# Kernel optimization log

Hardware: AMD Instinct MI355X
Metric: run time of the kernel (lower is better)

Reference implementation:

```python
import jax, jax.numpy as jnp
import numpy as np

B, S, D, H, E, K = 2, 1024, 1024, 4096, 8, 2
HE = 4 * D  # expert FFN inner dim
LN_EPS = 1e-5


def layernorm(x, g, b):
    m = x.mean(-1, keepdims=True)
    v = ((x - m) ** 2).mean(-1, keepdims=True)
    return (x - m) * jax.lax.rsqrt(v + LN_EPS) * g + b


def pos_encoding(S, D):
    pos = jnp.arange(S, dtype=jnp.float32)[:, None]
    i = jnp.arange(0, D, 2, dtype=jnp.float32)
    div = jnp.exp(-(jnp.log(10000.0)) * i / D)
    pe = jnp.zeros((S, D), dtype=jnp.float32)
    pe = pe.at[:, 0::2].set(jnp.sin(pos * div))
    pe = pe.at[:, 1::2].set(jnp.cos(pos * div))
    return pe


def setup_inputs() -> dict:
    key = jax.random.key(0)
    ks = jax.random.split(key, 16)
    w = lambda k, sh, s=0.02: (jax.random.normal(k, sh, dtype=jnp.float32) * s)
    return {
        "x": jax.random.normal(ks[0], (B, S, D), dtype=jnp.float32),
        # router: LayerNorm -> Linear(D,H) -> GELU -> Linear(H,E)
        "r_ln_g": jnp.ones((D,), jnp.float32), "r_ln_b": jnp.zeros((D,), jnp.float32),
        "r_w1": w(ks[1], (D, H)), "r_b1": jnp.zeros((H,), jnp.float32),
        "r_w2": w(ks[2], (H, E)), "r_b2": jnp.zeros((E,), jnp.float32),
        "temperature": jnp.ones((1,), jnp.float32) * 0.07,
        # stacked expert params: LayerNorm -> Linear(D,HE) -> GELU -> Linear(HE,D)
        "e_ln_g": jnp.ones((E, D), jnp.float32), "e_ln_b": jnp.zeros((E, D), jnp.float32),
        "e_w1": w(ks[3], (E, D, HE)), "e_b1": jnp.zeros((E, HE), jnp.float32),
        "e_w2": w(ks[4], (E, HE, D)), "e_b2": jnp.zeros((E, D), jnp.float32),
        # combiner: LayerNorm -> Linear(D,2D) -> GELU -> Linear(2D,D)
        "c_ln_g": jnp.ones((D,), jnp.float32), "c_ln_b": jnp.zeros((D,), jnp.float32),
        "c_w1": w(ks[5], (D, 2 * D)), "c_b1": jnp.zeros((2 * D,), jnp.float32),
        "c_w2": w(ks[6], (2 * D, D)), "c_b2": jnp.zeros((D,), jnp.float32),
        "o_ln_g": jnp.ones((D,), jnp.float32), "o_ln_b": jnp.zeros((D,), jnp.float32),
    }


def reference(x, r_ln_g, r_ln_b, r_w1, r_b1, r_w2, r_b2, temperature,
              e_ln_g, e_ln_b, e_w1, e_b1, e_w2, e_b2,
              c_ln_g, c_ln_b, c_w1, c_b1, c_w2, c_b2, o_ln_g, o_ln_b):
    gelu = lambda t: jax.nn.gelu(t, approximate=False)
    h = x + pos_encoding(S, D)[None]  # [B,S,D]
    # router logits with learned temperature
    r = layernorm(h, r_ln_g, r_ln_b)
    r = gelu(jnp.einsum("bsd,dh->bsh", r, r_w1) + r_b1)
    logits = (jnp.einsum("bsh,he->bse", r, r_w2) + r_b2) / temperature
    probs = jax.nn.softmax(logits, axis=-1)  # [B,S,E]
    topk_p, topk_i = jax.lax.top_k(probs, K)
    # sparse gate [B,S,E]: softmax prob on selected experts, 0 elsewhere
    gate = (jax.nn.one_hot(topk_i, E, dtype=probs.dtype) * topk_p[..., None]).sum(-2)
    # per-expert FFN on all tokens (dense reference of dispatch/compute/combine)
    m = h.mean(-1, keepdims=True)
    v = ((h - m) ** 2).mean(-1, keepdims=True)
    xhat = (h - m) * jax.lax.rsqrt(v + LN_EPS)  # [B,S,D], shared LN stats
    y = xhat[None] * e_ln_g[:, None, None, :] + e_ln_b[:, None, None, :]  # [E,B,S,D]
    f = gelu(jnp.einsum("ebsd,edh->ebsh", y, e_w1) + e_b1[:, None, None, :])
    f = jnp.einsum("ebsh,ehd->ebsd", f, e_w2) + e_b2[:, None, None, :]
    combined = jnp.einsum("bse,ebsd->bsd", gate, f)
    # expert combiner MLP + residual + output norm
    c = layernorm(combined, c_ln_g, c_ln_b)
    c = gelu(jnp.einsum("bsd,de->bse", c, c_w1) + c_b1)
    c = jnp.einsum("bse,ed->bsd", c, c_w2) + c_b2
    return layernorm(h + c, o_ln_g, o_ln_b)
```

## Files before the change

### kernel.cpp

```cpp
#include <hip/hip_runtime.h>
#include <stdint.h>

#define TOK 2048
#define DD  1024
#define RH  4096
#define HE  4096
#define NE  8
#define CH  2048
#define MAXTILE 40
#define MAXROWS 5120

using bf16x8 = __attribute__((ext_vector_type(8))) short;
using f32x4  = __attribute__((ext_vector_type(4))) float;

__device__ __forceinline__ unsigned short f2bf(float f) {
  union { float f; uint32_t u; } v; v.f = f;
  uint32_t r = (v.u + 0x7fffu + ((v.u >> 16) & 1u)) >> 16;
  return (unsigned short)r;
}
__device__ __forceinline__ float bf2f(unsigned short h) {
  union { uint32_t u; float f; } v; v.u = ((uint32_t)h) << 16;
  return v.f;
}
__device__ __forceinline__ float gelu_f(float x) {
  return 0.5f * x * (1.0f + erff(x * 0.70710678118654752440f));
}

#define GLD(SRC, DST) __builtin_amdgcn_global_load_lds( \
    (const __attribute__((address_space(1))) uint32_t*)(const void*)(SRC), \
    (__attribute__((address_space(3))) uint32_t*)(void*)(DST), 16, 0, 0)

__device__ __forceinline__ void block_ln_stats(float s1, float s2, float& mean, float& rstd) {
  #pragma unroll
  for (int off = 32; off > 0; off >>= 1) {
    s1 += __shfl_down(s1, off);
    s2 += __shfl_down(s2, off);
  }
  __shared__ float sh[8];
  int tid = threadIdx.x;
  if ((tid & 63) == 0) { sh[tid >> 6] = s1; sh[4 + (tid >> 6)] = s2; }
  __syncthreads();
  float t1 = sh[0] + sh[1] + sh[2] + sh[3];
  float t2 = sh[4] + sh[5] + sh[6] + sh[7];
  mean = t1 * (1.0f / 1024.0f);
  float var = t2 * (1.0f / 1024.0f) - mean * mean;
  rstd = rsqrtf(var + 1e-5f);
}

__global__ void k_prep(const float* __restrict__ x, float* __restrict__ h,
                       float* __restrict__ xh32, unsigned short* __restrict__ xhi,
                       unsigned short* __restrict__ xlo) {
  int t = blockIdx.x;
  int s = t & 1023;
  int tid = threadIdx.x;
  float4 xv = ((const float4*)(x + (size_t)t * DD))[tid];
  float v[4]; float s1 = 0.f, s2 = 0.f;
  #pragma unroll
  for (int k = 0; k < 4; ++k) {
    int d = tid * 4 + k;
    float xc = (k == 0) ? xv.x : (k == 1) ? xv.y : (k == 2) ? xv.z : xv.w;
    float i2 = (float)(d & ~1);
    float div = expf(-9.2103403719761836f * i2 * (1.0f / 1024.0f));
    float ang = (float)s * div;
    float pe = (d & 1) ? cosf(ang) : sinf(ang);
    float hv = xc + pe;
    v[k] = hv; s1 += hv; s2 += hv * hv;
  }
  float mean, rstd;
  block_ln_stats(s1, s2, mean, rstd);
  float4 ho; ho.x = v[0]; ho.y = v[1]; ho.z = v[2]; ho.w = v[3];
  ((float4*)(h + (size_t)t * DD))[tid] = ho;
  float xn[4]; unsigned short hh[4], ll[4];
  #pragma unroll
  for (int k = 0; k < 4; ++k) {
    xn[k] = (v[k] - mean) * rstd;
    hh[k] = f2bf(xn[k]);
    ll[k] = f2bf(xn[k] - bf2f(hh[k]));
  }
  float4 xo; xo.x = xn[0]; xo.y = xn[1]; xo.z = xn[2]; xo.w = xn[3];
  ((float4*)(xh32 + (size_t)t * DD))[tid] = xo;
  ushort4 h4; h4.x = hh[0]; h4.y = hh[1]; h4.z = hh[2]; h4.w = hh[3];
  ((ushort4*)(xhi + (size_t)t * DD))[tid] = h4;
  ushort4 l4; l4.x = ll[0]; l4.y = ll[1]; l4.z = ll[2]; l4.w = ll[3];
  ((ushort4*)(xlo + (size_t)t * DD))[tid] = l4;
}

__global__ void k_tconv(const float* __restrict__ in, const float* __restrict__ g,
                        unsigned short* __restrict__ out, int D, int N,
                        long long in_bs, long long g_bs, long long out_bs) {
  __shared__ float tile[32][33];
  int e = blockIdx.z;
  const float* inb = in + (size_t)e * in_bs;
  unsigned short* outb = out + (size_t)e * out_bs;
  int n0 = blockIdx.x * 32, d0 = blockIdx.y * 32;
  int tn = threadIdx.x & 31, tr = threadIdx.x >> 5;
  #pragma unroll
  for (int rr = 0; rr < 4; ++rr) {
    int dl = tr + rr * 8;
    float v = inb[(size_t)(d0 + dl) * N + n0 + tn];
    if (g) v *= g[(size_t)e * g_bs + d0 + dl];
    tile[dl][tn] = v;
  }
  __syncthreads();
  #pragma unroll
  for (int rr = 0; rr < 4; ++rr) {
    int nl = tr + rr * 8;
    outb[(size_t)(n0 + nl) * D + d0 + tn] = f2bf(tile[tn][nl]);
  }
}

__global__ void k_tconv_split(const float* __restrict__ in, const float* __restrict__ g,
                              unsigned short* __restrict__ oh, unsigned short* __restrict__ ol,
                              float* __restrict__ o32, int D, int N) {
  __shared__ float tile[32][33];
  int n0 = blockIdx.x * 32, d0 = blockIdx.y * 32;
  int tn = threadIdx.x & 31, tr = threadIdx.x >> 5;
  #pragma unroll
  for (int rr = 0; rr < 4; ++rr) {
    int dl = tr + rr * 8;
    float v = in[(size_t)(d0 + dl) * N + n0 + tn];
    if (g) v *= g[d0 + dl];
    tile[dl][tn] = v;
  }
  __syncthreads();
  #pragma unroll
  for (int rr = 0; rr < 4; ++rr) {
    int nl = tr + rr * 8;
    float v = tile[tn][nl];
    size_t off = (size_t)(n0 + nl) * D + d0 + tn;
    unsigned short hi = f2bf(v);
    oh[off] = hi;
    ol[off] = f2bf(v - bf2f(hi));
    o32[off] = v;
  }
}

__global__ void k_foldbias(const float* __restrict__ w, const float* __restrict__ lnb,
                           const float* __restrict__ b1, float* __restrict__ outb,
                           int D, int N, long long w_bs, long long lnb_bs,
                           long long b_bs, long long o_bs) {
  int e = blockIdx.y;
  int n = blockIdx.x * 256 + threadIdx.x;
  const float* wb = w + (size_t)e * w_bs;
  const float* lb = lnb + (size_t)e * lnb_bs;
  float acc = b1[(size_t)e * b_bs + n];
  for (int d = 0; d < D; ++d) {
    float l = lb[d];
    if (l != 0.f) acc += l * wb[(size_t)d * N + n];
  }
  outb[(size_t)e * o_bs + n] = acc;
}

template <int DO_GELU, int OUT_BF16>
__global__ __launch_bounds__(256)
void k_gemm(const unsigned short* __restrict__ A, const unsigned short* __restrict__ B,
            const float* __restrict__ bias, void* __restrict__ Cv, int N, int K,
            long long a_bs, long long b_bs, long long bias_bs, long long c_bs) {
  __shared__ __align__(16) unsigned short As[128 * 32];
  __shared__ __align__(16) unsigned short Bs[128 * 32];
  const int tid = threadIdx.x;
  const int w = tid >> 6, lane = tid & 63;
  const int q = lane >> 4, r16 = lane & 15;
  const int e = blockIdx.z;
  const int n0 = blockIdx.x * 128, m0 = blockIdx.y * 128;
  const unsigned short* Ab = A + (size_t)e * a_bs;
  const unsigned short* Bb = B + (size_t)e * b_bs;
  f32x4 acc[4][4];
  #pragma unroll
  for (int i = 0; i < 4; ++i)
    #pragma unroll
    for (int j = 0; j < 4; ++j) acc[i][j] = (f32x4){0.f, 0.f, 0.f, 0.f};
  const int srow = w * 32 + (lane >> 2);
  const int scol = (lane & 3) * 8;
  const unsigned short* a_src = Ab + (size_t)(m0 + srow) * K + scol;
  const unsigned short* b_src = Bb + (size_t)(n0 + srow) * K + scol;
  unsigned short* a_dst = &As[w * 1024];
  unsigned short* b_dst = &Bs[w * 1024];
  const int wm = w >> 1, wn = w & 1;
  for (int kt = 0; kt < K; kt += 32) {
    GLD(a_src + kt, a_dst);
    GLD(a_src + kt + (size_t)16 * K, a_dst + 512);
    GLD(b_src + kt, b_dst);
    GLD(b_src + kt + (size_t)16 * K, b_dst + 512);
    __syncthreads();
    bf16x8 af[4], bfv[4];
    #pragma unroll
    for (int i = 0; i < 4; ++i)
      af[i] = *(const bf16x8*)&As[(wm * 64 + i * 16 + r16) * 32 + q * 8];
    #pragma unroll
    for (int j = 0; j < 4; ++j)
      bfv[j] = *(const bf16x8*)&Bs[(wn * 64 + j * 16 + r16) * 32 + q * 8];
    #pragma unroll
    for (int i = 0; i < 4; ++i)
      #pragma unroll
      for (int j = 0; j < 4; ++j)
        acc[i][j] = __builtin_amdgcn_mfma_f32_16x16x32_bf16(af[i], bfv[j], acc[i][j], 0, 0, 0);
    __syncthreads();
  }
  #pragma unroll
  for (int j = 0; j < 4; ++j) {
    int col = n0 + wn * 64 + j * 16 + r16;
    float bv = bias[(size_t)e * bias_bs + col];
    #pragma unroll
    for (int i = 0; i < 4; ++i) {
      int row = m0 + wm * 64 + i * 16 + q * 4;
      #pragma unroll
      for (int t2 = 0; t2 < 4; ++t2) {
        float vv = acc[i][j][t2] + bv;
        if (DO_GELU) vv = gelu_f(vv);
        size_t off = (size_t)e * c_bs + (size_t)(row + t2) * N + col;
        if (OUT_BF16) ((unsigned short*)Cv)[off] = f2bf(vv);
        else ((float*)Cv)[off] = vv;
      }
    }
  }
}

__global__ __launch_bounds__(256)
void k_gemm_g1(const unsigned short* __restrict__ A, const unsigned short* __restrict__ W,
               const float* __restrict__ bias, unsigned short* __restrict__ C,
               const int* __restrict__ tok_of, const int* __restrict__ tile_e,
               const int* __restrict__ tile_r0, const int* __restrict__ ntiles) {
  if ((int)blockIdx.y >= *ntiles) return;
  __shared__ __align__(16) unsigned short As[128 * 32];
  __shared__ __align__(16) unsigned short Bs[128 * 32];
  const int tid = threadIdx.x;
  const int w = tid >> 6, lane = tid & 63;
  const int q = lane >> 4, r16 = lane & 15;
  const int e = tile_e[blockIdx.y];
  const int row0 = tile_r0[blockIdx.y];
  const int n0 = blockIdx.x * 128;
  f32x4 acc[4][4];
  #pragma unroll
  for (int i = 0; i < 4; ++i)
    #pragma unroll
    for (int j = 0; j < 4; ++j) acc[i][j] = (f32x4){0.f, 0.f, 0.f, 0.f};
  const int srow = w * 32 + (lane >> 2);
  const int scol = (lane & 3) * 8;
  const int t0 = tok_of[row0 + srow];
  const int t1 = tok_of[row0 + srow + 16];
  const unsigned short* a_src0 = A + (size_t)t0 * DD + scol;
  const unsigned short* a_src1 = A + (size_t)t1 * DD + scol;
  const unsigned short* b_src = W + (size_t)e * RH * DD + (size_t)(n0 + srow) * DD + scol;
  unsigned short* a_dst = &As[w * 1024];
  unsigned short* b_dst = &Bs[w * 1024];
  const int wm = w >> 1, wn = w & 1;
  for (int kt = 0; kt < DD; kt += 32) {
    GLD(a_src0 + kt, a_dst);
    GLD(a_src1 + kt, a_dst + 512);
    GLD(b_src + kt, b_dst);
    GLD(b_src + kt + (size_t)16 * DD, b_dst + 512);
    __syncthreads();
    bf16x8 af[4], bfv[4];
    #pragma unroll
    for (int i = 0; i < 4; ++i)
      af[i] = *(const bf16x8*)&As[(wm * 64 + i * 16 + r16) * 32 + q * 8];
    #pragma unroll
    for (int j = 0; j < 4; ++j)
      bfv[j] = *(const bf16x8*)&Bs[(wn * 64 + j * 16 + r16) * 32 + q * 8];
    #pragma unroll
    for (int i = 0; i < 4; ++i)
      #pragma unroll
      for (int j = 0; j < 4; ++j)
        acc[i][j] = __builtin_amdgcn_mfma_f32_16x16x32_bf16(af[i], bfv[j], acc[i][j], 0, 0, 0);
    __syncthreads();
  }
  #pragma unroll
  for (int j = 0; j < 4; ++j) {
    int col = n0 + wn * 64 + j * 16 + r16;
    float bv = bias[(size_t)e * RH + col];
    #pragma unroll
    for (int i = 0; i < 4; ++i) {
      int row = row0 + wm * 64 + i * 16 + q * 4;
      #pragma unroll
      for (int t2 = 0; t2 < 4; ++t2)
        C[(size_t)(row + t2) * RH + col] = f2bf(gelu_f(acc[i][j][t2] + bv));
    }
  }
}

__global__ __launch_bounds__(256)
void k_gemm_g2(const unsigned short* __restrict__ A, const unsigned short* __restrict__ W,
               unsigned short* __restrict__ C, const int* __restrict__ tile_e,
               const int* __restrict__ tile_r0, const int* __restrict__ ntiles) {
  if ((int)blockIdx.y >= *ntiles) return;
  __shared__ __align__(16) unsigned short As[128 * 32];
  __shared__ __align__(16) unsigned short Bs[128 * 32];
  const int tid = threadIdx.x;
  const int w = tid >> 6, lane = tid & 63;
  const int q = lane >> 4, r16 = lane & 15;
  const int e = tile_e[blockIdx.y];
  const int row0 = tile_r0[blockIdx.y];
  const int n0 = blockIdx.x * 128;
  f32x4 acc[4][4];
  #pragma unroll
  for (int i = 0; i < 4; ++i)
    #pragma unroll
    for (int j = 0; j < 4; ++j) acc[i][j] = (f32x4){0.f, 0.f, 0.f, 0.f};
  const int srow = w * 32 + (lane >> 2);
  const int scol = (lane & 3) * 8;
  const unsigned short* a_src = A + (size_t)(row0 + srow) * HE + scol;
  const unsigned short* b_src = W + (size_t)e * DD * HE + (size_t)(n0 + srow) * HE + scol;
  unsigned short* a_dst = &As[w * 1024];
  unsigned short* b_dst = &Bs[w * 1024];
  const int wm = w >> 1, wn = w & 1;
  for (int kt = 0; kt < HE; kt += 32) {
    GLD(a_src + kt, a_dst);
    GLD(a_src + kt + (size_t)16 * HE, a_dst + 512);
    GLD(b_src + kt, b_dst);
    GLD(b_src + kt + (size_t)16 * HE, b_dst + 512);
    __syncthreads();
    bf16x8 af[4], bfv[4];
    #pragma unroll
    for (int i = 0; i < 4; ++i)
      af[i] = *(const bf16x8*)&As[(wm * 64 + i * 16 + r16) * 32 + q * 8];
    #pragma unroll
    for (int j = 0; j < 4; ++j)
      bfv[j] = *(const bf16x8*)&Bs[(wn * 64 + j * 16 + r16) * 32 + q * 8];
    #pragma unroll
    for (int i = 0; i < 4; ++i)
      #pragma unroll
      for (int j = 0; j < 4; ++j)
        acc[i][j] = __builtin_amdgcn_mfma_f32_16x16x32_bf16(af[i], bfv[j], acc[i][j], 0, 0, 0);
    __syncthreads();
  }
  #pragma unroll
  for (int j = 0; j < 4; ++j) {
    int col = n0 + wn * 64 + j * 16 + r16;
    #pragma unroll
    for (int i = 0; i < 4; ++i) {
      int row = row0 + wm * 64 + i * 16 + q * 4;
      #pragma unroll
      for (int t2 = 0; t2 < 4; ++t2)
        C[(size_t)(row + t2) * DD + col] = f2bf(acc[i][j][t2]);
    }
  }
}

__global__ __launch_bounds__(256)
void k_gemm_split(const unsigned short* __restrict__ Ah, const unsigned short* __restrict__ Al,
                  const unsigned short* __restrict__ Bh, const unsigned short* __restrict__ Bl,
                  const float* __restrict__ bias, float* __restrict__ C, int N, int K) {
  __shared__ __align__(16) unsigned short Ahs[128 * 32];
  __shared__ __align__(16) unsigned short Als[128 * 32];
  __shared__ __align__(16) unsigned short Bhs[128 * 32];
  __shared__ __align__(16) unsigned short Bls[128 * 32];
  const int tid = threadIdx.x;
  const int w = tid >> 6, lane = tid & 63;
  const int q = lane >> 4, r16 = lane & 15;
  const int n0 = blockIdx.x * 128, m0 = blockIdx.y * 128;
  f32x4 acc[4][4];
  #pragma unroll
  for (int i = 0; i < 4; ++i)
    #pragma unroll
    for (int j = 0; j < 4; ++j) acc[i][j] = (f32x4){0.f, 0.f, 0.f, 0.f};
  const int srow = w * 32 + (lane >> 2);
  const int scol = (lane & 3) * 8;
  const unsigned short* ah_src = Ah + (size_t)(m0 + srow) * K + scol;
  const unsigned short* al_src = Al + (size_t)(m0 + srow) * K + scol;
  const unsigned short* bh_src = Bh + (size_t)(n0 + srow) * K + scol;
  const unsigned short* bl_src = Bl + (size_t)(n0 + srow) * K + scol;
  const int wm = w >> 1, wn = w & 1;
  for (int kt = 0; kt < K; kt += 32) {
    GLD(ah_src + kt, &Ahs[w * 1024]);
    GLD(ah_src + kt + (size_t)16 * K, &Ahs[w * 1024 + 512]);
    GLD(al_src + kt, &Als[w * 1024]);
    GLD(al_src + kt + (size_t)16 * K, &Als[w * 1024 + 512]);
    GLD(bh_src + kt, &Bhs[w * 1024]);
    GLD(bh_src + kt + (size_t)16 * K, &Bhs[w * 1024 + 512]);
    GLD(bl_src + kt, &Bls[w * 1024]);
    GLD(bl_src + kt + (size_t)16 * K, &Bls[w * 1024 + 512]);
    __syncthreads();
    bf16x8 ah[4], al[4], bh[4], bl[4];
    #pragma unroll
    for (int i = 0; i < 4; ++i) {
      int o = (wm * 64 + i * 16 + r16) * 32 + q * 8;
      ah[i] = *(const bf16x8*)&Ahs[o];
      al[i] = *(const bf16x8*)&Als[o];
    }
    #pragma unroll
    for (int j = 0; j < 4; ++j) {
      int o = (wn * 64 + j * 16 + r16) * 32 + q * 8;
      bh[j] = *(const bf16x8*)&Bhs[o];
      bl[j] = *(const bf16x8*)&Bls[o];
    }
    #pragma unroll
    for (int i = 0; i < 4; ++i)
      #pragma unroll
      for (int j = 0; j < 4; ++j) {
        acc[i][j] = __builtin_amdgcn_mfma_f32_16x16x32_bf16(ah[i], bh[j], acc[i][j], 0, 0, 0);
        acc[i][j] = __builtin_amdgcn_mfma_f32_16x16x32_bf16(al[i], bh[j], acc[i][j], 0, 0, 0);
        acc[i][j] = __builtin_amdgcn_mfma_f32_16x16x32_bf16(ah[i], bl[j], acc[i][j], 0, 0, 0);
      }
    __syncthreads();
  }
  #pragma unroll
  for (int j = 0; j < 4; ++j) {
    int col = n0 + wn * 64 + j * 16 + r16;
    float bv = bias[col];
    #pragma unroll
    for (int i = 0; i < 4; ++i) {
      int row = m0 + wm * 64 + i * 16 + q * 4;
      #pragma unroll
      for (int t2 = 0; t2 < 4; ++t2)
        C[(size_t)(row + t2) * N + col] = gelu_f(acc[i][j][t2] + bv);
    }
  }
}

__global__ void k_logits(const float* __restrict__ r, const float* __restrict__ w2,
                         const float* __restrict__ b2, const float* __restrict__ temp,
                         int* __restrict__ sel_i, float* __restrict__ sel_p,
                         int* __restrict__ flag, float* __restrict__ lg32) {
  int t = blockIdx.x, tid = threadIdx.x;
  const float* rr = r + (size_t)t * RH;
  float acc[NE];
  #pragma unroll
  for (int e = 0; e < NE; ++e) acc[e] = 0.f;
  #pragma unroll
  for (int k4 = 0; k4 < 4; ++k4) {
    float4 rv4 = ((const float4*)rr)[tid * 4 + k4];
    #pragma unroll
    for (int kk = 0; kk < 4; ++kk) {
      int d = tid * 16 + k4 * 4 + kk;
      float rv = (kk == 0) ? rv4.x : (kk == 1) ? rv4.y : (kk == 2) ? rv4.z : rv4.w;
      const float4* wr = (const float4*)(w2 + (size_t)d * NE);
      float4 w0 = wr[0], w1 = wr[1];
      acc[0] += rv * w0.x; acc[1] += rv * w0.y; acc[2] += rv * w0.z; acc[3] += rv * w0.w;
      acc[4] += rv * w1.x; acc[5] += rv * w1.y; acc[6] += rv * w1.z; acc[7] += rv * w1.w;
    }
  }
  #pragma unroll
  for (int off = 32; off > 0; off >>= 1)
    #pragma unroll
    for (int e = 0; e < NE; ++e) acc[e] += __shfl_down(acc[e], off);
  __shared__ float shl[4][NE];
  int w = tid >> 6, lane = tid & 63;
  if (lane == 0) {
    #pragma unroll
    for (int e = 0; e < NE; ++e) shl[w][e] = acc[e];
  }
  __syncthreads();
  if (tid == 0) {
    float tmp = temp[0];
    float lg[NE];
    #pragma unroll
    for (int e = 0; e < NE; ++e)
      lg[e] = (shl[0][e] + shl[1][e] + shl[2][e] + shl[3][e] + b2[e]) / tmp;
    float mx = lg[0];
    for (int e = 1; e < NE; ++e) mx = fmaxf(mx, lg[e]);
    float p[NE], se = 0.f;
    for (int e = 0; e < NE; ++e) { p[e] = expf(lg[e] - mx); se += p[e]; }
    float inv = 1.f / se;
    int i1 = 0; float p1 = p[0];
    for (int e = 1; e < NE; ++e) if (p[e] > p1) { p1 = p[e]; i1 = e; }
    int i2 = -1; float p2 = -1.f;
    for (int e = 0; e < NE; ++e) if (e != i1 && p[e] > p2) { p2 = p[e]; i2 = e; }
    sel_i[t * 2] = i1; sel_i[t * 2 + 1] = i2;
    sel_p[t * 2] = p1 * inv; sel_p[t * 2 + 1] = p2 * inv;
    float a1 = -1e30f, a2 = -1e30f, a3 = -1e30f;
    for (int e = 0; e < NE; ++e) {
      float vv = lg[e];
      if (vv > a1) { a3 = a2; a2 = a1; a1 = vv; }
      else if (vv > a2) { a3 = a2; a2 = vv; }
      else if (vv > a3) a3 = vv;
    }
    int fl = (a2 - a3 < 0.01f) ? 1 : 0;
    flag[t] = fl;
    if (fl) {
      #pragma unroll
      for (int e = 0; e < NE; ++e) lg32[(size_t)t * NE + e] = 0.f;
    }
  }
}

__global__ void k_triage2(const int* __restrict__ flag, const float* __restrict__ xh32,
                          const float* __restrict__ W32, const float* __restrict__ biasr,
                          const float* __restrict__ w2, float* __restrict__ lg32) {
  int t = blockIdx.y;
  if (flag[t] == 0) return;
  int tid = threadIdx.x;
  int w = tid >> 6, lane = tid & 63;
  __shared__ float xs[DD];
  ((float4*)xs)[tid] = ((const float4*)(xh32 + (size_t)t * DD))[tid];
  __syncthreads();
  int hh0 = blockIdx.x * 64 + w * 16;
  float acc[NE];
  #pragma unroll
  for (int e = 0; e < NE; ++e) acc[e] = 0.f;
  #pragma unroll
  for (int r = 0; r < 16; ++r) {
    int hh = hh0 + r;
    const float4* wrow = (const float4*)(W32 + (size_t)hh * DD);
    float s = 0.f;
    #pragma unroll
    for (int c = 0; c < 4; ++c) {
      float4 wv = wrow[lane + 64 * c];
      float4 xv = ((const float4*)xs)[lane + 64 * c];
      s += wv.x * xv.x + wv.y * xv.y + wv.z * xv.z + wv.w * xv.w;
    }
    #pragma unroll
    for (int off = 32; off > 0; off >>= 1) s += __shfl_down(s, off);
    if (lane == 0) {
      float r1 = gelu_f(s + biasr[hh]);
      const float* wr = w2 + (size_t)hh * NE;
      #pragma unroll
      for (int e = 0; e < NE; ++e) acc[e] += r1 * wr[e];
    }
  }
  __shared__ float sh2[4][NE];
  if (lane == 0) {
    #pragma unroll
    for (int e = 0; e < NE; ++e) sh2[w][e] = acc[e];
  }
  __syncthreads();
  if (tid < NE) {
    float v = sh2[0][tid] + sh2[1][tid] + sh2[2][tid] + sh2[3][tid];
    atomicAdd(&lg32[(size_t)t * NE + tid], v);
  }
}

__global__ void k_gate2(const int* __restrict__ flag, const float* __restrict__ lg32,
                        const float* __restrict__ b2, const float* __restrict__ temp,
                        int* __restrict__ sel_i, float* __restrict__ sel_p) {
  int t = blockIdx.x * 256 + threadIdx.x;
  if (t >= TOK || flag[t] == 0) return;
  float tmp = temp[0];
  float lg[NE];
  #pragma unroll
  for (int e = 0; e < NE; ++e) lg[e] = (lg32[(size_t)t * NE + e] + b2[e]) / tmp;
  float mx = lg[0];
  for (int e = 1; e < NE; ++e) mx = fmaxf(mx, lg[e]);
  float p[NE], se = 0.f;
  for (int e = 0; e < NE; ++e) { p[e] = expf(lg[e] - mx); se += p[e]; }
  float inv = 1.f / se;
  int i1 = 0; float p1 = p[0];
  for (int e = 1; e < NE; ++e) if (p[e] > p1) { p1 = p[e]; i1 = e; }
  int i2 = -1; float p2 = -1.f;
  for (int e = 0; e < NE; ++e) if (e != i1 && p[e] > p2) { p2 = p[e]; i2 = e; }
  sel_i[t * 2] = i1; sel_i[t * 2 + 1] = i2;
  sel_p[t * 2] = p1 * inv; sel_p[t * 2 + 1] = p2 * inv;
}

__global__ void k_count(const int* __restrict__ sel_i, int* __restrict__ cnt) {
  int t = blockIdx.x * 256 + threadIdx.x;
  if (t >= TOK) return;
  atomicAdd(&cnt[sel_i[2 * t]], 1);
  atomicAdd(&cnt[sel_i[2 * t + 1]], 1);
}

__global__ void k_offsets(const int* __restrict__ cnt, int* __restrict__ off,
                          int* __restrict__ tile_e, int* __restrict__ tile_r0,
                          int* __restrict__ ntiles) {
  if (threadIdx.x == 0) {
    int cur = 0, nt = 0;
    for (int e = 0; e < NE; ++e) {
      off[e] = cur;
      int n = (cnt[e] + 127) >> 7;
      for (int k = 0; k < n; ++k) { tile_e[nt] = e; tile_r0[nt] = cur + 128 * k; nt++; }
      cur += n * 128;
    }
    *ntiles = nt;
  }
}

__global__ void k_fill(const int* __restrict__ sel_i, const int* __restrict__ off,
                       int* __restrict__ fill, int* __restrict__ slotarr,
                       int* __restrict__ tok_of) {
  int t = blockIdx.x * 256 + threadIdx.x;
  if (t >= TOK) return;
  #pragma unroll
  for (int j = 0; j < 2; ++j) {
    int e = sel_i[2 * t + j];
    int pos = atomicAdd(&fill[e], 1);
    int s = off[e] + pos;
    slotarr[2 * t + j] = s;
    tok_of[s] = t;
  }
}

__global__ void k_combine2(const int* __restrict__ slotarr, const int* __restrict__ sel_i,
                           const float* __restrict__ sel_p, const unsigned short* __restrict__ pairout,
                           const float* __restrict__ e_b2, unsigned short* __restrict__ xc) {
  int t = blockIdx.x, tid = threadIdx.x;
  int s0 = slotarr[t * 2], s1 = slotarr[t * 2 + 1];
  int e0 = sel_i[t * 2], e1 = sel_i[t * 2 + 1];
  float w0 = sel_p[t * 2], w1 = sel_p[t * 2 + 1];
  ushort4 u0 = ((const ushort4*)(pairout + (size_t)s0 * DD))[tid];
  ushort4 u1 = ((const ushort4*)(pairout + (size_t)s1 * DD))[tid];
  float4 b0 = ((const float4*)(e_b2 + (size_t)e0 * DD))[tid];
  float4 b1v = ((const float4*)(e_b2 + (size_t)e1 * DD))[tid];
  float v[4];
  v[0] = w0 * (bf2f(u0.x) + b0.x) + w1 * (bf2f(u1.x) + b1v.x);
  v[1] = w0 * (bf2f(u0.y) + b0.y) + w1 * (bf2f(u1.y) + b1v.y);
  v[2] = w0 * (bf2f(u0.z) + b0.z) + w1 * (bf2f(u1.z) + b1v.z);
  v[3] = w0 * (bf2f(u0.w) + b0.w) + w1 * (bf2f(u1.w) + b1v.w);
  float s1f = v[0] + v[1] + v[2] + v[3];
  float s2f = v[0]*v[0] + v[1]*v[1] + v[2]*v[2] + v[3]*v[3];
  float mean, rstd;
  block_ln_stats(s1f, s2f, mean, rstd);
  ushort4 o;
  o.x = f2bf((v[0] - mean) * rstd); o.y = f2bf((v[1] - mean) * rstd);
  o.z = f2bf((v[2] - mean) * rstd); o.w = f2bf((v[3] - mean) * rstd);
  ((ushort4*)(xc + (size_t)t * DD))[tid] = o;
}

__global__ void k_final(const float* __restrict__ h, const unsigned short* __restrict__ c2,
                        const float* __restrict__ og, const float* __restrict__ ob,
                        float* __restrict__ out) {
  int t = blockIdx.x, tid = threadIdx.x;
  float4 hv = ((const float4*)(h + (size_t)t * DD))[tid];
  ushort4 cu = ((const ushort4*)(c2 + (size_t)t * DD))[tid];
  float v[4] = {hv.x + bf2f(cu.x), hv.y + bf2f(cu.y), hv.z + bf2f(cu.z), hv.w + bf2f(cu.w)};
  float s1 = v[0] + v[1] + v[2] + v[3];
  float s2 = v[0]*v[0] + v[1]*v[1] + v[2]*v[2] + v[3]*v[3];
  float mean, rstd;
  block_ln_stats(s1, s2, mean, rstd);
  float4 gv = ((const float4*)og)[tid];
  float4 bv = ((const float4*)ob)[tid];
  float4 o;
  o.x = (v[0] - mean) * rstd * gv.x + bv.x;
  o.y = (v[1] - mean) * rstd * gv.y + bv.y;
  o.z = (v[2] - mean) * rstd * gv.z + bv.z;
  o.w = (v[3] - mean) * rstd * gv.w + bv.w;
  ((float4*)(out + (size_t)t * DD))[tid] = o;
}

extern "C" void kernel_launch(void* const* d_in, const int* in_sizes, int n_in,
                              void* d_out, int out_size, void* d_ws, size_t ws_size,
                              hipStream_t stream) {
  (void)in_sizes; (void)n_in; (void)out_size; (void)ws_size;
  const float* x      = (const float*)d_in[0];
  const float* r_ln_g = (const float*)d_in[1];
  const float* r_ln_b = (const float*)d_in[2];
  const float* r_w1   = (const float*)d_in[3];
  const float* r_b1   = (const float*)d_in[4];
  const float* r_w2   = (const float*)d_in[5];
  const float* r_b2   = (const float*)d_in[6];
  const float* temp   = (const float*)d_in[7];
  const float* e_ln_g = (const float*)d_in[8];
  const float* e_ln_b = (const float*)d_in[9];
  const float* e_w1   = (const float*)d_in[10];
  const float* e_b1   = (const float*)d_in[11];
  const float* e_w2   = (const float*)d_in[12];
  const float* e_b2   = (const float*)d_in[13];
  const float* c_ln_g = (const float*)d_in[14];
  const float* c_ln_b = (const float*)d_in[15];
  const float* c_w1   = (const float*)d_in[16];
  const float* c_b1   = (const float*)d_in[17];
  const float* c_w2   = (const float*)d_in[18];
  const float* c_b2   = (const float*)d_in[19];
  const float* o_ln_g = (const float*)d_in[20];
  const float* o_ln_b = (const float*)d_in[21];
  float* out = (float*)d_out;

  char* base = (char*)d_ws;
  long long cur = 0;
  auto take = [&](long long sz) { char* r = base + cur; cur += (sz + 255) & ~255LL; return r; };

  float* h      = (float*)take(8388608);
  float* xh32   = (float*)take(8388608);
  unsigned short* xhi = (unsigned short*)take(4194304);
  unsigned short* xlo = (unsigned short*)take(4194304);
  unsigned short* WrH = (unsigned short*)take(8388608);
  unsigned short* WrL = (unsigned short*)take(8388608);
  float* Wr32   = (float*)take(16777216);
  float* biasr  = (float*)take(16384);
  float* ract   = (float*)take(33554432);
  int*   flag   = (int*)take(8192);
  float* lg32   = (float*)take(65536);
  int*   sel_i  = (int*)take(16384);
  float* sel_p  = (float*)take(16384);
  int*   cnt    = (int*)take(256);
  int*   off    = (int*)take(256);
  int*   fillc  = (int*)take(256);
  int*   tile_e = (int*)take(256);
  int*   tile_r0= (int*)take(256);
  int*   ntiles = (int*)take(256);
  int*   slotarr= (int*)take(16384);
  int*   tok_of = (int*)take(MAXROWS * 4);
  unsigned short* We1 = (unsigned short*)take(67108864);
  float* be1    = (float*)take(131072);
  unsigned short* We2 = (unsigned short*)take(67108864);
  unsigned short* Wc1 = (unsigned short*)take(4194304);
  float* bc1    = (float*)take(8192);
  unsigned short* Wc2 = (unsigned short*)take(4194304);
  unsigned short* xc  = (unsigned short*)take(4194304);
  unsigned short* c1  = (unsigned short*)take(8388608);
  unsigned short* c2  = (unsigned short*)take(4194304);
  unsigned short* F1g = (unsigned short*)take((long long)MAXROWS * RH * 2);
  unsigned short* pairout = (unsigned short*)take((long long)MAXROWS * DD * 2);

  hipMemsetAsync(cnt, 0, 256, stream);
  hipMemsetAsync(fillc, 0, 256, stream);
  hipMemsetAsync(tok_of, 0, MAXROWS * 4, stream);

  k_prep<<<TOK, 256, 0, stream>>>(x, h, xh32, xhi, xlo);
  k_tconv_split<<<dim3(RH/32, DD/32, 1), 256, 0, stream>>>(r_w1, r_ln_g, WrH, WrL, Wr32, DD, RH);
  k_tconv<<<dim3(RH/32, DD/32, NE), 256, 0, stream>>>(e_w1, e_ln_g, We1, DD, RH,
      (long long)DD*RH, (long long)DD, (long long)RH*DD);
  k_tconv<<<dim3(DD/32, HE/32, NE), 256, 0, stream>>>(e_w2, nullptr, We2, HE, DD,
      (long long)HE*DD, 0LL, (long long)DD*HE);
  k_tconv<<<dim3(CH/32, DD/32, 1), 256, 0, stream>>>(c_w1, c_ln_g, Wc1, DD, CH, 0LL, 0LL, 0LL);
  k_tconv<<<dim3(DD/32, CH/32, 1), 256, 0, stream>>>(c_w2, nullptr, Wc2, CH, DD, 0LL, 0LL, 0LL);
  k_foldbias<<<dim3(RH/256, 1), 256, 0, stream>>>(r_w1, r_ln_b, r_b1, biasr, DD, RH, 0LL, 0LL, 0LL, 0LL);
  k_foldbias<<<dim3(RH/256, NE), 256, 0, stream>>>(e_w1, e_ln_b, e_b1, be1, DD, RH,
      (long long)DD*RH, (long long)DD, (long long)RH, (long long)RH);
  k_foldbias<<<dim3(CH/256, 1), 256, 0, stream>>>(c_w1, c_ln_b, c_b1, bc1, DD, CH, 0LL, 0LL, 0LL, 0LL);

  k_gemm_split<<<dim3(RH/128, TOK/128, 1), 256, 0, stream>>>(xhi, xlo, WrH, WrL, biasr, ract, RH, DD);
  k_logits<<<TOK, 256, 0, stream>>>(ract, r_w2, r_b2, temp, sel_i, sel_p, flag, lg32);
  k_triage2<<<dim3(RH/64, TOK), 256, 0, stream>>>(flag, xh32, Wr32, biasr, r_w2, lg32);
  k_gate2<<<TOK/256, 256, 0, stream>>>(flag, lg32, r_b2, temp, sel_i, sel_p);

  k_count<<<TOK/256, 256, 0, stream>>>(sel_i, cnt);
  k_offsets<<<1, 64, 0, stream>>>(cnt, off, tile_e, tile_r0, ntiles);
  k_fill<<<TOK/256, 256, 0, stream>>>(sel_i, off, fillc, slotarr, tok_of);

  k_gemm_g1<<<dim3(RH/128, MAXTILE), 256, 0, stream>>>(xhi, We1, be1, F1g,
      tok_of, tile_e, tile_r0, ntiles);
  k_gemm_g2<<<dim3(DD/128, MAXTILE), 256, 0, stream>>>(F1g, We2, pairout,
      tile_e, tile_r0, ntiles);

  k_combine2<<<TOK, 256, 0, stream>>>(slotarr, sel_i, sel_p, pairout, e_b2, xc);
  k_gemm<1,1><<<dim3(CH/128, TOK/128, 1), 256, 0, stream>>>(xc, Wc1, bc1, (void*)c1, CH, DD, 0LL, 0LL, 0LL, 0LL);
  k_gemm<0,1><<<dim3(DD/128, TOK/128, 1), 256, 0, stream>>>(c1, Wc2, c_b2, (void*)c2, DD, CH, 0LL, 0LL, 0LL, 0LL);
  k_final<<<TOK, 256, 0, stream>>>(h, c2, o_ln_g, o_ln_b, out);
}
```

Before: 1.092 ms.

## Split-K the expert down-proj and combiner GEMMs, compact triage, widen transposes

Adds split-K to the expert second GEMM (4 slices) and to both combiner GEMMs (2 and 4 slices). Each slice writes fp32 partials, which are summed in the consumer kernels (combine2, a new GELU reduce kernel, and final). The router triage now builds a compacted list of flagged tokens instead of launching one block row per token, and the weight transpose kernel uses 64x64 tiles with vectorized loads and stores. The aim is to fill more CUs on GEMMs whose grids are small and to avoid launching thousands of idle triage blocks. The cost is extra fp32 partial traffic, plus reuse of the WrH and biasr buffers as scratch, which relies on their size being sufficient.

```diff
diff --git a/kernel.cpp b/kernel.cpp
--- a/kernel.cpp
+++ b/kernel.cpp
@@ -9,6 +9,9 @@
 #define CH  2048
 #define MAXTILE 40
 #define MAXROWS 5120
+#define KSG2 4
+#define KSC1 2
+#define KSC2 4
 
 using bf16x8 = __attribute__((ext_vector_type(8))) short;
 using f32x4  = __attribute__((ext_vector_type(4))) float;
@@ -88,24 +91,34 @@
 __global__ void k_tconv(const float* __restrict__ in, const float* __restrict__ g,
                         unsigned short* __restrict__ out, int D, int N,
                         long long in_bs, long long g_bs, long long out_bs) {
-  __shared__ float tile[32][33];
+  __shared__ float tile[64][65];
   int e = blockIdx.z;
   const float* inb = in + (size_t)e * in_bs;
   unsigned short* outb = out + (size_t)e * out_bs;
-  int n0 = blockIdx.x * 32, d0 = blockIdx.y * 32;
-  int tn = threadIdx.x & 31, tr = threadIdx.x >> 5;
+  int n0 = blockIdx.x * 64, d0 = blockIdx.y * 64;
+  int c4 = threadIdx.x & 15;
+  int r0 = threadIdx.x >> 4;
   #pragma unroll
   for (int rr = 0; rr < 4; ++rr) {
-    int dl = tr + rr * 8;
-    float v = inb[(size_t)(d0 + dl) * N + n0 + tn];
-    if (g) v *= g[(size_t)e * g_bs + d0 + dl];
-    tile[dl][tn] = v;
+    int dl = r0 + rr * 16;
+    float4 v = *(const float4*)(inb + (size_t)(d0 + dl) * N + n0 + c4 * 4);
+    if (g) {
+      float gv = g[(size_t)e * g_bs + d0 + dl];
+      v.x *= gv; v.y *= gv; v.z *= gv; v.w *= gv;
+    }
+    tile[dl][c4 * 4 + 0] = v.x; tile[dl][c4 * 4 + 1] = v.y;
+    tile[dl][c4 * 4 + 2] = v.z; tile[dl][c4 * 4 + 3] = v.w;
   }
   __syncthreads();
+  int q = threadIdx.x & 15;
+  int nb = threadIdx.x >> 4;
   #pragma unroll
   for (int rr = 0; rr < 4; ++rr) {
-    int nl = tr + rr * 8;
-    outb[(size_t)(n0 + nl) * D + d0 + tn] = f2bf(tile[tn][nl]);
+    int nl = nb + rr * 16;
+    ushort4 o;
+    o.x = f2bf(tile[q * 4 + 0][nl]); o.y = f2bf(tile[q * 4 + 1][nl]);
+    o.z = f2bf(tile[q * 4 + 2][nl]); o.w = f2bf(tile[q * 4 + 3][nl]);
+    *(ushort4*)(outb + (size_t)(n0 + nl) * D + d0 + q * 4) = o;
   }
 }
 
@@ -151,20 +164,16 @@
   outb[(size_t)e * o_bs + n] = acc;
 }
 
-template <int DO_GELU, int OUT_BF16>
 __global__ __launch_bounds__(256)
-void k_gemm(const unsigned short* __restrict__ A, const unsigned short* __restrict__ B,
-            const float* __restrict__ bias, void* __restrict__ Cv, int N, int K,
-            long long a_bs, long long b_bs, long long bias_bs, long long c_bs) {
+void k_gemm_sk(const unsigned short* __restrict__ A, const unsigned short* __restrict__ B,
+               float* __restrict__ C, int N, int K, int kslice, long long c_slice) {
   __shared__ __align__(16) unsigned short As[128 * 32];
   __shared__ __align__(16) unsigned short Bs[128 * 32];
   const int tid = threadIdx.x;
   const int w = tid >> 6, lane = tid & 63;
   const int q = lane >> 4, r16 = lane & 15;
-  const int e = blockIdx.z;
+  const int kz = blockIdx.z;
   const int n0 = blockIdx.x * 128, m0 = blockIdx.y * 128;
-  const unsigned short* Ab = A + (size_t)e * a_bs;
-  const unsigned short* Bb = B + (size_t)e * b_bs;
   f32x4 acc[4][4];
   #pragma unroll
   for (int i = 0; i < 4; ++i)
@@ -172,12 +181,12 @@
     for (int j = 0; j < 4; ++j) acc[i][j] = (f32x4){0.f, 0.f, 0.f, 0.f};
   const int srow = w * 32 + (lane >> 2);
   const int scol = (lane & 3) * 8;
-  const unsigned short* a_src = Ab + (size_t)(m0 + srow) * K + scol;
-  const unsigned short* b_src = Bb + (size_t)(n0 + srow) * K + scol;
+  const unsigned short* a_src = A + (size_t)(m0 + srow) * K + scol + (size_t)kz * kslice;
+  const unsigned short* b_src = B + (size_t)(n0 + srow) * K + scol + (size_t)kz * kslice;
   unsigned short* a_dst = &As[w * 1024];
   unsigned short* b_dst = &Bs[w * 1024];
   const int wm = w >> 1, wn = w & 1;
-  for (int kt = 0; kt < K; kt += 32) {
+  for (int kt = 0; kt < kslice; kt += 32) {
     GLD(a_src + kt, a_dst);
     GLD(a_src + kt + (size_t)16 * K, a_dst + 512);
     GLD(b_src + kt, b_dst);
@@ -200,20 +209,30 @@
   #pragma unroll
   for (int j = 0; j < 4; ++j) {
     int col = n0 + wn * 64 + j * 16 + r16;
-    float bv = bias[(size_t)e * bias_bs + col];
     #pragma unroll
     for (int i = 0; i < 4; ++i) {
       int row = m0 + wm * 64 + i * 16 + q * 4;
       #pragma unroll
-      for (int t2 = 0; t2 < 4; ++t2) {
-        float vv = acc[i][j][t2] + bv;
-        if (DO_GELU) vv = gelu_f(vv);
-        size_t off = (size_t)e * c_bs + (size_t)(row + t2) * N + col;
-        if (OUT_BF16) ((unsigned short*)Cv)[off] = f2bf(vv);
-        else ((float*)Cv)[off] = vv;
-      }
-    }
-  }
+      for (int t2 = 0; t2 < 4; ++t2)
+        C[(size_t)kz * c_slice + (size_t)(row + t2) * N + col] = acc[i][j][t2];
+    }
+  }
+}
+
+__global__ void k_redg(const float* __restrict__ p, const float* __restrict__ bias,
+                       unsigned short* __restrict__ o, int N, long long slice, int nsl) {
+  size_t i = ((size_t)blockIdx.x * 256 + threadIdx.x) * 4;
+  float4 a = *(const float4*)(p + i);
+  for (int s = 1; s < nsl; ++s) {
+    float4 b = *(const float4*)(p + (size_t)s * slice + i);
+    a.x += b.x; a.y += b.y; a.z += b.z; a.w += b.w;
+  }
+  int col = (int)(i & (size_t)(N - 1));
+  float4 bv = *(const float4*)(bias + col);
+  ushort4 u;
+  u.x = f2bf(gelu_f(a.x + bv.x)); u.y = f2bf(gelu_f(a.y + bv.y));
+  u.z = f2bf(gelu_f(a.z + bv.z)); u.w = f2bf(gelu_f(a.w + bv.w));
+  *(ushort4*)(o + i) = u;
 }
 
 __global__ __launch_bounds__(256)
@@ -281,7 +300,7 @@
 
 __global__ __launch_bounds__(256)
 void k_gemm_g2(const unsigned short* __restrict__ A, const unsigned short* __restrict__ W,
-               unsigned short* __restrict__ C, const int* __restrict__ tile_e,
+               float* __restrict__ C, const int* __restrict__ tile_e,
                const int* __restrict__ tile_r0, const int* __restrict__ ntiles) {
   if ((int)blockIdx.y >= *ntiles) return;
   __shared__ __align__(16) unsigned short As[128 * 32];
@@ -292,6 +311,7 @@
   const int e = tile_e[blockIdx.y];
   const int row0 = tile_r0[blockIdx.y];
   const int n0 = blockIdx.x * 128;
+  const int kz = blockIdx.z;
   f32x4 acc[4][4];
   #pragma unroll
   for (int i = 0; i < 4; ++i)
@@ -299,12 +319,13 @@
     for (int j = 0; j < 4; ++j) acc[i][j] = (f32x4){0.f, 0.f, 0.f, 0.f};
   const int srow = w * 32 + (lane >> 2);
   const int scol = (lane & 3) * 8;
-  const unsigned short* a_src = A + (size_t)(row0 + srow) * HE + scol;
-  const unsigned short* b_src = W + (size_t)e * DD * HE + (size_t)(n0 + srow) * HE + scol;
+  const unsigned short* a_src = A + (size_t)(row0 + srow) * HE + scol + (size_t)kz * (HE / KSG2);
+  const unsigned short* b_src = W + (size_t)e * DD * HE + (size_t)(n0 + srow) * HE + scol
+                                + (size_t)kz * (HE / KSG2);
   unsigned short* a_dst = &As[w * 1024];
   unsigned short* b_dst = &Bs[w * 1024];
   const int wm = w >> 1, wn = w & 1;
-  for (int kt = 0; kt < HE; kt += 32) {
+  for (int kt = 0; kt < HE / KSG2; kt += 32) {
     GLD(a_src + kt, a_dst);
     GLD(a_src + kt + (size_t)16 * HE, a_dst + 512);
     GLD(b_src + kt, b_dst);
@@ -332,7 +353,7 @@
       int row = row0 + wm * 64 + i * 16 + q * 4;
       #pragma unroll
       for (int t2 = 0; t2 < 4; ++t2)
-        C[(size_t)(row + t2) * DD + col] = f2bf(acc[i][j][t2]);
+        C[(size_t)kz * MAXROWS * DD + (size_t)(row + t2) * DD + col] = acc[i][j][t2];
     }
   }
 }
@@ -474,49 +495,59 @@
   }
 }
 
-__global__ void k_triage2(const int* __restrict__ flag, const float* __restrict__ xh32,
-                          const float* __restrict__ W32, const float* __restrict__ biasr,
-                          const float* __restrict__ w2, float* __restrict__ lg32) {
-  int t = blockIdx.y;
-  if (flag[t] == 0) return;
+__global__ void k_flaglist(const int* __restrict__ flag, int* __restrict__ ftok,
+                           int* __restrict__ nflag) {
+  int t = blockIdx.x * 256 + threadIdx.x;
+  if (t >= TOK) return;
+  if (flag[t]) { int p = atomicAdd(nflag, 1); ftok[p] = t; }
+}
+
+__global__ void k_triage2(const int* __restrict__ nflag, const int* __restrict__ ftok,
+                          const float* __restrict__ xh32, const float* __restrict__ W32,
+                          const float* __restrict__ biasr, const float* __restrict__ w2,
+                          float* __restrict__ lg32) {
+  int nf = *nflag;
+  __shared__ float xs[DD];
+  __shared__ float sh2[4][NE];
   int tid = threadIdx.x;
   int w = tid >> 6, lane = tid & 63;
-  __shared__ float xs[DD];
-  ((float4*)xs)[tid] = ((const float4*)(xh32 + (size_t)t * DD))[tid];
-  __syncthreads();
-  int hh0 = blockIdx.x * 64 + w * 16;
-  float acc[NE];
-  #pragma unroll
-  for (int e = 0; e < NE; ++e) acc[e] = 0.f;
-  #pragma unroll
-  for (int r = 0; r < 16; ++r) {
-    int hh = hh0 + r;
-    const float4* wrow = (const float4*)(W32 + (size_t)hh * DD);
-    float s = 0.f;
-    #pragma unroll
-    for (int c = 0; c < 4; ++c) {
-      float4 wv = wrow[lane + 64 * c];
-      float4 xv = ((const float4*)xs)[lane + 64 * c];
-      s += wv.x * xv.x + wv.y * xv.y + wv.z * xv.z + wv.w * xv.w;
-    }
-    #pragma unroll
-    for (int off = 32; off > 0; off >>= 1) s += __shfl_down(s, off);
+  for (int idx = blockIdx.y; idx < nf; idx += (int)gridDim.y) {
+    int t = ftok[idx];
+    ((float4*)xs)[tid] = ((const float4*)(xh32 + (size_t)t * DD))[tid];
+    __syncthreads();
+    int hh0 = blockIdx.x * 64 + w * 16;
+    float acc[NE];
+    #pragma unroll
+    for (int e = 0; e < NE; ++e) acc[e] = 0.f;
+    #pragma unroll
+    for (int r = 0; r < 16; ++r) {
+      int hh = hh0 + r;
+      const float4* wrow = (const float4*)(W32 + (size_t)hh * DD);
+      float s = 0.f;
+      #pragma unroll
+      for (int c = 0; c < 4; ++c) {
+        float4 wv = wrow[lane + 64 * c];
+        float4 xv = ((const float4*)xs)[lane + 64 * c];
+        s += wv.x * xv.x + wv.y * xv.y + wv.z * xv.z + wv.w * xv.w;
+      }
+      #pragma unroll
+      for (int off = 32; off > 0; off >>= 1) s += __shfl_down(s, off);
+      if (lane == 0) {
+        float r1 = gelu_f(s + biasr[hh]);
+        const float* wr = w2 + (size_t)hh * NE;
+        #pragma unroll
+        for (int e = 0; e < NE; ++e) acc[e] += r1 * wr[e];
+      }
+    }
     if (lane == 0) {
-      float r1 = gelu_f(s + biasr[hh]);
-      const float* wr = w2 + (size_t)hh * NE;
-      #pragma unroll
-      for (int e = 0; e < NE; ++e) acc[e] += r1 * wr[e];
-    }
-  }
-  __shared__ float sh2[4][NE];
-  if (lane == 0) {
-    #pragma unroll
-    for (int e = 0; e < NE; ++e) sh2[w][e] = acc[e];
-  }
-  __syncthreads();
-  if (tid < NE) {
-    float v = sh2[0][tid] + sh2[1][tid] + sh2[2][tid] + sh2[3][tid];
-    atomicAdd(&lg32[(size_t)t * NE + tid], v);
+      #pragma unroll
+      for (int e = 0; e < NE; ++e) sh2[w][e] = acc[e];
+    }
+    __syncthreads();
+    if (tid < NE) {
+      float v = sh2[0][tid] + sh2[1][tid] + sh2[2][tid] + sh2[3][tid];
+      atomicAdd(&lg32[(size_t)t * NE + tid], v);
+    }
   }
 }
 
@@ -580,21 +611,28 @@
 }
 
 __global__ void k_combine2(const int* __restrict__ slotarr, const int* __restrict__ sel_i,
-                           const float* __restrict__ sel_p, const unsigned short* __restrict__ pairout,
+                           const float* __restrict__ sel_p, const float* __restrict__ pairpart,
                            const float* __restrict__ e_b2, unsigned short* __restrict__ xc) {
   int t = blockIdx.x, tid = threadIdx.x;
   int s0 = slotarr[t * 2], s1 = slotarr[t * 2 + 1];
   int e0 = sel_i[t * 2], e1 = sel_i[t * 2 + 1];
   float w0 = sel_p[t * 2], w1 = sel_p[t * 2 + 1];
-  ushort4 u0 = ((const ushort4*)(pairout + (size_t)s0 * DD))[tid];
-  ushort4 u1 = ((const ushort4*)(pairout + (size_t)s1 * DD))[tid];
+  float a0x = 0.f, a0y = 0.f, a0z = 0.f, a0w = 0.f;
+  float a1x = 0.f, a1y = 0.f, a1z = 0.f, a1w = 0.f;
+  #pragma unroll
+  for (int z = 0; z < KSG2; ++z) {
+    float4 u = ((const float4*)(pairpart + (size_t)z * MAXROWS * DD + (size_t)s0 * DD))[tid];
+    a0x += u.x; a0y += u.y; a0z += u.z; a0w += u.w;
+    float4 v = ((const float4*)(pairpart + (size_t)z * MAXROWS * DD + (size_t)s1 * DD))[tid];
+    a1x += v.x; a1y += v.y; a1z += v.z; a1w += v.w;
+  }
   float4 b0 = ((const float4*)(e_b2 + (size_t)e0 * DD))[tid];
   float4 b1v = ((const float4*)(e_b2 + (size_t)e1 * DD))[tid];
   float v[4];
-  v[0] = w0 * (bf2f(u0.x) + b0.x) + w1 * (bf2f(u1.x) + b1v.x);
-  v[1] = w0 * (bf2f(u0.y) + b0.y) + w1 * (bf2f(u1.y) + b1v.y);
-  v[2] = w0 * (bf2f(u0.z) + b0.z) + w1 * (bf2f(u1.z) + b1v.z);
-  v[3] = w0 * (bf2f(u0.w) + b0.w) + w1 * (bf2f(u1.w) + b1v.w);
+  v[0] = w0 * (a0x + b0.x) + w1 * (a1x + b1v.x);
+  v[1] = w0 * (a0y + b0.y) + w1 * (a1y + b1v.y);
+  v[2] = w0 * (a0z + b0.z) + w1 * (a1z + b1v.z);
+  v[3] = w0 * (a0w + b0.w) + w1 * (a1w + b1v.w);
   float s1f = v[0] + v[1] + v[2] + v[3];
   float s2f = v[0]*v[0] + v[1]*v[1] + v[2]*v[2] + v[3]*v[3];
   float mean, rstd;
@@ -605,13 +643,19 @@
   ((ushort4*)(xc + (size_t)t * DD))[tid] = o;
 }
 
-__global__ void k_final(const float* __restrict__ h, const unsigned short* __restrict__ c2,
-                        const float* __restrict__ og, const float* __restrict__ ob,
-                        float* __restrict__ out) {
+__global__ void k_final(const float* __restrict__ h, const float* __restrict__ c2p,
+                        const float* __restrict__ cb2, const float* __restrict__ og,
+                        const float* __restrict__ ob, float* __restrict__ out) {
   int t = blockIdx.x, tid = threadIdx.x;
   float4 hv = ((const float4*)(h + (size_t)t * DD))[tid];
-  ushort4 cu = ((const ushort4*)(c2 + (size_t)t * DD))[tid];
-  float v[4] = {hv.x + bf2f(cu.x), hv.y + bf2f(cu.y), hv.z + bf2f(cu.z), hv.w + bf2f(cu.w)};
+  float ax = 0.f, ay = 0.f, az = 0.f, aw = 0.f;
+  #pragma unroll
+  for (int z = 0; z < KSC2; ++z) {
+    float4 u = ((const float4*)(c2p + (size_t)z * TOK * DD + (size_t)t * DD))[tid];
+    ax += u.x; ay += u.y; az += u.z; aw += u.w;
+  }
+  float4 cb = ((const float4*)cb2)[tid];
+  float v[4] = {hv.x + ax + cb.x, hv.y + ay + cb.y, hv.z + az + cb.z, hv.w + aw + cb.w};
   float s1 = v[0] + v[1] + v[2] + v[3];
   float s2 = v[0]*v[0] + v[1]*v[1] + v[2]*v[2] + v[3]*v[3];
   float mean, rstd;
@@ -677,6 +721,8 @@
   int*   tile_e = (int*)take(256);
   int*   tile_r0= (int*)take(256);
   int*   ntiles = (int*)take(256);
+  int*   nflag  = (int*)take(256);
+  int*   ftok   = (int*)take(TOK * 4);
   int*   slotarr= (int*)take(16384);
   int*   tok_of = (int*)take(MAXROWS * 4);
   unsigned short* We1 = (unsigned short*)take(67108864);
@@ -687,22 +733,24 @@
   unsigned short* Wc2 = (unsigned short*)take(4194304);
   unsigned short* xc  = (unsigned short*)take(4194304);
   unsigned short* c1  = (unsigned short*)take(8388608);
-  unsigned short* c2  = (unsigned short*)take(4194304);
   unsigned short* F1g = (unsigned short*)take((long long)MAXROWS * RH * 2);
-  unsigned short* pairout = (unsigned short*)take((long long)MAXROWS * DD * 2);
+  float* pairpart = (float*)take((long long)KSG2 * MAXROWS * DD * 4);
+  float* c1part = (float*)WrH;
+  float* c2part = (float*)biasr;
 
   hipMemsetAsync(cnt, 0, 256, stream);
   hipMemsetAsync(fillc, 0, 256, stream);
+  hipMemsetAsync(nflag, 0, 256, stream);
   hipMemsetAsync(tok_of, 0, MAXROWS * 4, stream);
 
   k_prep<<<TOK, 256, 0, stream>>>(x, h, xh32, xhi, xlo);
   k_tconv_split<<<dim3(RH/32, DD/32, 1), 256, 0, stream>>>(r_w1, r_ln_g, WrH, WrL, Wr32, DD, RH);
-  k_tconv<<<dim3(RH/32, DD/32, NE), 256, 0, stream>>>(e_w1, e_ln_g, We1, DD, RH,
+  k_tconv<<<dim3(RH/64, DD/64, NE), 256, 0, stream>>>(e_w1, e_ln_g, We1, DD, RH,
       (long long)DD*RH, (long long)DD, (long long)RH*DD);
-  k_tconv<<<dim3(DD/32, HE/32, NE), 256, 0, stream>>>(e_w2, nullptr, We2, HE, DD,
+  k_tconv<<<dim3(DD/64, HE/64, NE), 256, 0, stream>>>(e_w2, nullptr, We2, HE, DD,
       (long long)HE*DD, 0LL, (long long)DD*HE);
-  k_tconv<<<dim3(CH/32, DD/32, 1), 256, 0, stream>>>(c_w1, c_ln_g, Wc1, DD, CH, 0LL, 0LL, 0LL);
-  k_tconv<<<dim3(DD/32, CH/32, 1), 256, 0, stream>>>(c_w2, nullptr, Wc2, CH, DD, 0LL, 0LL, 0LL);
+  k_tconv<<<dim3(CH/64, DD/64, 1), 256, 0, stream>>>(c_w1, c_ln_g, Wc1, DD, CH, 0LL, 0LL, 0LL);
+  k_tconv<<<dim3(DD/64, CH/64, 1), 256, 0, stream>>>(c_w2, nullptr, Wc2, CH, DD, 0LL, 0LL, 0LL);
   k_foldbias<<<dim3(RH/256, 1), 256, 0, stream>>>(r_w1, r_ln_b, r_b1, biasr, DD, RH, 0LL, 0LL, 0LL, 0LL);
   k_foldbias<<<dim3(RH/256, NE), 256, 0, stream>>>(e_w1, e_ln_b, e_b1, be1, DD, RH,
       (long long)DD*RH, (long long)DD, (long long)RH, (long long)RH);
@@ -710,7 +758,8 @@
 
   k_gemm_split<<<dim3(RH/128, TOK/128, 1), 256, 0, stream>>>(xhi, xlo, WrH, WrL, biasr, ract, RH, DD);
   k_logits<<<TOK, 256, 0, stream>>>(ract, r_w2, r_b2, temp, sel_i, sel_p, flag, lg32);
-  k_triage2<<<dim3(RH/64, TOK), 256, 0, stream>>>(flag, xh32, Wr32, biasr, r_w2, lg32);
+  k_flaglist<<<TOK/256, 256, 0, stream>>>(flag, ftok, nflag);
+  k_triage2<<<dim3(RH/64, 32), 256, 0, stream>>>(nflag, ftok, xh32, Wr32, biasr, r_w2, lg32);
   k_gate2<<<TOK/256, 256, 0, stream>>>(flag, lg32, r_b2, temp, sel_i, sel_p);
 
   k_count<<<TOK/256, 256, 0, stream>>>(sel_i, cnt);
@@ -719,11 +768,14 @@
 
   k_gemm_g1<<<dim3(RH/128, MAXTILE), 256, 0, stream>>>(xhi, We1, be1, F1g,
       tok_of, tile_e, tile_r0, ntiles);
-  k_gemm_g2<<<dim3(DD/128, MAXTILE), 256, 0, stream>>>(F1g, We2, pairout,
+  k_gemm_g2<<<dim3(DD/128, MAXTILE, KSG2), 256, 0, stream>>>(F1g, We2, pairpart,
       tile_e, tile_r0, ntiles);
 
-  k_combine2<<<TOK, 256, 0, stream>>>(slotarr, sel_i, sel_p, pairout, e_b2, xc);
-  k_gemm<1,1><<<dim3(CH/128, TOK/128, 1), 256, 0, stream>>>(xc, Wc1, bc1, (void*)c1, CH, DD, 0LL, 0LL, 0LL, 0LL);
-  k_gemm<0,1><<<dim3(DD/128, TOK/128, 1), 256, 0, stream>>>(c1, Wc2, c_b2, (void*)c2, DD, CH, 0LL, 0LL, 0LL, 0LL);
-  k_final<<<TOK, 256, 0, stream>>>(h, c2, o_ln_g, o_ln_b, out);
-}
+  k_combine2<<<TOK, 256, 0, stream>>>(slotarr, sel_i, sel_p, pairpart, e_b2, xc);
+  k_gemm_sk<<<dim3(CH/128, TOK/128, KSC1), 256, 0, stream>>>(xc, Wc1, c1part, CH, DD,
+      DD/KSC1, (long long)TOK * CH);
+  k_redg<<<(TOK * CH) / 1024, 256, 0, stream>>>(c1part, bc1, c1, CH, (long long)TOK * CH, KSC1);
+  k_gemm_sk<<<dim3(DD/128, TOK/128, KSC2), 256, 0, stream>>>(c1, Wc2, c2part, DD, CH,
+      CH/KSC2, (long long)TOK * DD);
+  k_final<<<TOK, 256, 0, stream>>>(h, c2part, c_b2, o_ln_g, o_ln_b, out);
+}
```

Measured after the change: 1.097 ms. Within noise of the previous version (+0.5%).
